# Kernel optimization log

Measured on AMD Instinct MI355X. Metric: run time of the kernel, lower is better.

Reference implementation:

```python
import jax, jax.numpy as jnp
import numpy as np

N = 4096      # number of nodes (seq_len); > 1000 so dag positional encoding is skipped
IN = 45       # input_dim
HID = 256     # hidden_dim
NH = 4        # num_heads
DH = HID // NH
E = 131072    # edges (avg degree 32)
# bucketed time bias: (lo, hi, weight)
BUCKETS = ((0.0, 5.0, 0.2), (5.0, 15.0, 0.1), (15.0, 60.0, 0.0), (60.0, 240.0, -0.1))
NEG = -1e9


def setup_inputs() -> dict:
    key = jax.random.key(0)
    ks = jax.random.split(key, 16)

    def lin_w(k, fan_in, fan_out):
        return (jax.random.normal(k, (fan_in, fan_out), jnp.float32) / np.float32(np.sqrt(fan_in)))

    return {
        "node_features": jax.random.normal(ks[0], (N, IN), jnp.float32),
        "temporal_data": jax.random.uniform(ks[1], (N, N, 2), jnp.float32) * 300.0,  # dt minutes in [0,300)
        "edge_index": jax.random.randint(ks[2], (2, E), 0, N),
        "W_in": lin_w(ks[3], IN, HID), "b_in": jnp.zeros((HID,), jnp.float32),
        "Wq": lin_w(ks[4], HID, HID), "bq": jnp.zeros((HID,), jnp.float32),
        "Wk": lin_w(ks[5], HID, HID), "bk": jnp.zeros((HID,), jnp.float32),
        "Wv": lin_w(ks[6], HID, HID), "bv": jnp.zeros((HID,), jnp.float32),
        "Wo": lin_w(ks[7], HID, HID), "bo": jnp.zeros((HID,), jnp.float32),
    }


def reference(node_features, temporal_data, edge_index, W_in, b_in, Wq, bq, Wk, bk, Wv, bv, Wo, bo):
    L = node_features.shape[0]
    x = node_features @ W_in + b_in                      # [L, HID]; pos-enc skipped since L > 1000

    def heads(W, b):
        return (x @ W + b).reshape(L, NH, DH).transpose(1, 0, 2)  # [NH, L, DH]

    q, k, v = heads(Wq, bq), heads(Wk, bk), heads(Wv, bv)

    scores = jnp.einsum('hld,hsd->hls', q, k) / np.float32(np.sqrt(DH))  # [NH, L, L]

    # bucketed time bias from dt_minutes
    dt = temporal_data[:, :, 0]
    tb = jnp.zeros_like(dt)
    for lo, hi, w in BUCKETS:
        tb = tb + np.float32(w) * ((dt >= lo) & (dt <= hi)).astype(dt.dtype)
    scores = scores + tb[None]                           # broadcast over heads

    # edge mask: True blocks attention; edges and self-loops allowed
    u, vdst = edge_index[0], edge_index[1]
    block = jnp.ones((L, L), dtype=bool).at[u, vdst].set(False)
    diag = jnp.arange(L)
    block = block.at[diag, diag].set(False)
    scores = jnp.where(block[None], NEG, scores)

    attn = jax.nn.softmax(scores, axis=-1)               # eval mode: no dropout
    out = jnp.einsum('hls,hsd->hld', attn, v)            # [NH, L, DH]
    out = out.transpose(1, 0, 2).reshape(L, HID)         # [L, HID]
    return out @ Wo + bo
```

## Files before the change

### kernel.cpp

```cpp
#include <hip/hip_runtime.h>
#include <hip/hip_bf16.h>
#include <stdint.h>

#define N_NODES 4096
#define HIDDEN 256
#define NHEAD 4
#define DHEAD 64
#define NEDGE 131072
#define MASK_WORDS 128
#define KIN 64
#define MAXDEG 1024

typedef __attribute__((ext_vector_type(8))) short bf16x8;
typedef __attribute__((ext_vector_type(4))) float f32x4;
typedef __hip_bfloat16 bf16;

__device__ __forceinline__ float b2f(unsigned short s) {
    union { float f; unsigned u; } x;
    x.u = ((unsigned)s) << 16;
    return x.f;
}
__device__ __forceinline__ unsigned short f2bu(float f) {
    bf16 b = __float2bfloat16(f);
    return *(unsigned short*)&b;
}

__global__ __launch_bounds__(256) void prep_kernel(
    const float* __restrict__ nf,
    const float* __restrict__ W_in, const float* __restrict__ b_in,
    const float* __restrict__ Wq, const float* __restrict__ bq,
    const float* __restrict__ Wk, const float* __restrict__ bk,
    const float* __restrict__ Wv, const float* __restrict__ bv,
    const float* __restrict__ Wo,
    unsigned int* __restrict__ mask, bf16* __restrict__ nfp,
    bf16* __restrict__ WqkvT, float* __restrict__ bqkv,
    bf16* __restrict__ WoT)
{
    int t = blockIdx.x * 256 + threadIdx.x;
    if (t < 131072) {
        ((uint4*)mask)[t] = make_uint4(0, 0, 0, 0);
        return;
    }
    t -= 131072;
    if (t < N_NODES * KIN) {
        int row = t >> 6, c = t & 63;
        float v = (c < 45) ? nf[row * 45 + c] : 0.f;
        nfp[t] = __float2bfloat16(v);
        return;
    }
    t -= N_NODES * KIN;
    if (t < 3 * 256 * KIN) {
        int which = t >> 14, r = t & 16383;
        int n = r & 255, kk = r >> 8;
        const float* W = (which == 0) ? Wq : (which == 1) ? Wk : Wv;
        float dot = 0.f;
        if (kk < 45) {
            const float* wrow = W_in + kk * 256;
            for (int c = 0; c < 256; ++c)
                dot += wrow[c] * W[c * 256 + n];
        }
        WqkvT[(size_t)which * 16384 + (size_t)n * KIN + kk] = __float2bfloat16(dot);
        return;
    }
    t -= 3 * 256 * KIN;
    if (t < 3 * 256) {
        int which = t >> 8, n = t & 255;
        const float* W = (which == 0) ? Wq : (which == 1) ? Wk : Wv;
        const float* b = (which == 0) ? bq : (which == 1) ? bk : bv;
        float acc = b[n];
        for (int c = 0; c < 256; ++c)
            acc += b_in[c] * W[c * 256 + n];
        bqkv[t] = acc;
        return;
    }
    t -= 3 * 256;
    if (t < 65536) {
        int kk = t >> 8, n = t & 255;
        WoT[(size_t)n * 256 + kk] = __float2bfloat16(Wo[(size_t)kk * 256 + n]);
    }
}

template <bool OUT_BF16>
__device__ __forceinline__ void gemm_body(
    const bf16* __restrict__ A, const bf16* __restrict__ Bt,
    const float* __restrict__ bias, void* __restrict__ Cv,
    int K, int m_base, int n0)
{
    const int lane = threadIdx.x & 63;
    const int row = lane & 15, quad = lane >> 4;
    f32x4 acc0 = {0.f, 0.f, 0.f, 0.f};
    f32x4 acc1 = {0.f, 0.f, 0.f, 0.f};
    const short* Ap = (const short*)A;
    const short* Bp = (const short*)Bt;

    for (int k0 = 0; k0 < K; k0 += 32) {
        bf16x8 b  = *(const bf16x8*)(Bp + (size_t)(n0 + row) * K + k0 + quad * 8);
        bf16x8 a0 = *(const bf16x8*)(Ap + (size_t)(m_base + row) * K + k0 + quad * 8);
        bf16x8 a1 = *(const bf16x8*)(Ap + (size_t)(m_base + 16 + row) * K + k0 + quad * 8);
        acc0 = __builtin_amdgcn_mfma_f32_16x16x32_bf16(a0, b, acc0, 0, 0, 0);
        acc1 = __builtin_amdgcn_mfma_f32_16x16x32_bf16(a1, b, acc1, 0, 0, 0);
    }

    const int col = row;
    const float bval = bias[n0 + col];
#pragma unroll
    for (int e = 0; e < 4; ++e) {
        int m0 = m_base + quad * 4 + e;
        int m1 = m0 + 16;
        float v0 = acc0[e] + bval;
        float v1 = acc1[e] + bval;
        if (OUT_BF16) {
            ((bf16*)Cv)[(size_t)m0 * HIDDEN + n0 + col] = __float2bfloat16(v0);
            ((bf16*)Cv)[(size_t)m1 * HIDDEN + n0 + col] = __float2bfloat16(v1);
        } else {
            ((float*)Cv)[(size_t)m0 * HIDDEN + n0 + col] = v0;
            ((float*)Cv)[(size_t)m1 * HIDDEN + n0 + col] = v1;
        }
    }
}

__global__ __launch_bounds__(256) void qkv_scatter_kernel(
    const bf16* __restrict__ nfp, const bf16* __restrict__ WqkvT,
    const float* __restrict__ bqkv, const int* __restrict__ eidx,
    float* __restrict__ q, bf16* __restrict__ k, bf16* __restrict__ v,
    unsigned int* __restrict__ mask)
{
    int bx = blockIdx.x;
    if (bx < 1536) {
        int ntile = bx >> 5, mrow = bx & 31;
        int which = ntile >> 4;
        const bf16* Bt = WqkvT + (size_t)which * 16384;
        const float* bias = bqkv + which * 256;
        int wave = threadIdx.x >> 6;
        int mb = mrow * 128 + wave * 32;
        int n0 = (ntile & 15) * 16;
        if (which == 0)      gemm_body<false>(nfp, Bt, bias, q, KIN, mb, n0);
        else if (which == 1) gemm_body<true>(nfp, Bt, bias, k, KIN, mb, n0);
        else                 gemm_body<true>(nfp, Bt, bias, v, KIN, mb, n0);
        return;
    }
    int t = (bx - 1536) * 256 + threadIdx.x;
    if (t < NEDGE) {
        int u = eidx[t], w = eidx[NEDGE + t];
        atomicOr(&mask[u * MASK_WORDS + (w >> 5)], 1u << (w & 31));
    } else {
        int i = t - NEDGE;
        if (i < N_NODES)
            atomicOr(&mask[i * MASK_WORDS + (i >> 5)], 1u << (i & 31));
    }
}

__global__ __launch_bounds__(256) void attn_kernel(
    const float* __restrict__ q, const bf16* __restrict__ k,
    const bf16* __restrict__ v, const float* __restrict__ temporal,
    const unsigned int* __restrict__ mask, bf16* __restrict__ att)
{
    __shared__ int jlist[MAXDEG];
    __shared__ float qs[HIDDEN];
    __shared__ float pj[NHEAD][64];
    __shared__ int cnt;
    const int i = blockIdx.x, tid = threadIdx.x;

    if (tid == 0) cnt = 0;
    qs[tid] = q[(size_t)i * HIDDEN + tid];
    __syncthreads();
    if (tid < MASK_WORDS) {
        unsigned int bits = mask[(size_t)i * MASK_WORDS + tid];
        int n = __popc(bits);
        if (n) {
            int pos = atomicAdd(&cnt, n);
            while (bits) {
                int b = __ffs(bits) - 1;
                bits &= bits - 1;
                if (pos < MAXDEG) jlist[pos] = (tid << 5) + b;
                ++pos;
            }
        }
    }
    __syncthreads();
    const int nn = cnt;

    const int h = tid >> 6, lane = tid & 63;
    const int half = lane >> 5, dpair = lane & 31;
    const float* trow = temporal + (size_t)i * N_NODES * 2;
    const unsigned short* kp = (const unsigned short*)k;
    const unsigned short* vp = (const unsigned short*)v;
    const float* qh = qs + h * DHEAD;

    float l = 0.f, acc0 = 0.f, acc1 = 0.f;

    for (int c0 = 0; c0 < nn; c0 += 64) {
        const int cend = min(64, nn - c0);
        float s = -3.0e38f;
        if (lane < cend) {
            int j = jlist[c0 + lane];
            float dt = trow[(size_t)j * 2];
            const unsigned short* krow = kp + (size_t)j * HIDDEN + h * DHEAD;
            bf16x8 k8[8];
#pragma unroll
            for (int t = 0; t < 8; ++t)
                k8[t] = *(const bf16x8*)(krow + t * 8);
            float dot = 0.f;
#pragma unroll
            for (int t = 0; t < 8; ++t)
#pragma unroll
                for (int e = 0; e < 8; ++e)
                    dot += b2f((unsigned short)k8[t][e]) * qh[t * 8 + e];
            float tb = 0.f;
            tb += 0.2f * (float)((dt >= 0.f)  & (dt <= 5.f));
            tb += 0.1f * (float)((dt >= 5.f)  & (dt <= 15.f));
            tb -= 0.1f * (float)((dt >= 60.f) & (dt <= 240.f));
            s = dot * 0.125f + tb;
        }
        float p = __expf(s);
        float csum = p;
#pragma unroll
        for (int off = 32; off >= 1; off >>= 1)
            csum += __shfl_xor(csum, off, 64);
        pj[h][lane] = p;
        l += csum;
        for (int u0 = 0; u0 < cend; u0 += 8) {
#pragma unroll
            for (int t = 0; t < 4; ++t) {
                int idx = u0 + 2 * t + half;
                bool valid = idx < cend;
                int j = jlist[c0 + (valid ? idx : 0)];
                float pv = valid ? pj[h][idx] : 0.f;
                const unsigned short* vrow = vp + (size_t)j * HIDDEN + h * DHEAD + dpair * 2;
                ushort2 v2 = *(const ushort2*)vrow;
                acc0 += pv * b2f(v2.x);
                acc1 += pv * b2f(v2.y);
            }
        }
    }

    acc0 += __shfl_xor(acc0, 32, 64);
    acc1 += __shfl_xor(acc1, 32, 64);
    if (half == 0) {
        ushort2 o;
        o.x = f2bu(acc0 / l);
        o.y = f2bu(acc1 / l);
        *(ushort2*)((unsigned short*)att + (size_t)i * HIDDEN + h * DHEAD + dpair * 2) = o;
    }
}

__global__ __launch_bounds__(256) void gemm_out_kernel(
    const bf16* __restrict__ att, const bf16* __restrict__ WoT,
    const float* __restrict__ bo, float* __restrict__ out)
{
    int wave = threadIdx.x >> 6;
    gemm_body<false>(att, WoT, bo, out, HIDDEN,
                     blockIdx.y * 128 + wave * 32, blockIdx.x * 16);
}

extern "C" void kernel_launch(void* const* d_in, const int* in_sizes, int n_in,
                              void* d_out, int out_size, void* d_ws, size_t ws_size,
                              hipStream_t stream) {
    const float* nf       = (const float*)d_in[0];
    const float* temporal = (const float*)d_in[1];
    const int*   eidx     = (const int*)  d_in[2];
    const float* W_in     = (const float*)d_in[3];
    const float* b_in     = (const float*)d_in[4];
    const float* Wq       = (const float*)d_in[5];
    const float* bq       = (const float*)d_in[6];
    const float* Wk       = (const float*)d_in[7];
    const float* bk       = (const float*)d_in[8];
    const float* Wv       = (const float*)d_in[9];
    const float* bv       = (const float*)d_in[10];
    const float* Wo       = (const float*)d_in[11];
    const float* bo       = (const float*)d_in[12];
    float* out = (float*)d_out;

    char* ws = (char*)d_ws;
    const size_t MiB = 1 << 20, KiB = 1 << 10;
    unsigned int* mask = (unsigned int*)(ws);
    bf16*  nfp   = (bf16*)(ws + 2 * MiB);
    bf16*  WqkvT = (bf16*)(ws + 2 * MiB + 512 * KiB);
    float* bqkv  = (float*)(ws + 2 * MiB + 640 * KiB);
    bf16*  WoT   = (bf16*)(ws + 3 * MiB);
    float* q     = (float*)(ws + 4 * MiB);
    bf16*  kb    = (bf16*)(ws + 8 * MiB);
    bf16*  vb    = (bf16*)(ws + 10 * MiB);
    bf16*  att   = (bf16*)(ws + 12 * MiB);

    {
        int total = 131072 + N_NODES * KIN + 3 * 256 * KIN + 3 * 256 + 65536;
        prep_kernel<<<(total + 255) / 256, 256, 0, stream>>>(
            nf, W_in, b_in, Wq, bq, Wk, bk, Wv, bv, Wo,
            mask, nfp, WqkvT, bqkv, WoT);
    }

    qkv_scatter_kernel<<<1536 + 528, 256, 0, stream>>>(
        nfp, WqkvT, bqkv, eidx, q, kb, vb, mask);

    attn_kernel<<<N_NODES, 256, 0, stream>>>(q, kb, vb, temporal, mask, att);

    gemm_out_kernel<<<dim3(16, 32), 256, 0, stream>>>(att, WoT, bo, out);
}
```

Measured before the change: 247.2 us.

## Restructure attention to one wave per query row, store Q as bf16

The attention kernel now gives each wavefront its own query row, four rows per block, instead of spreading one row across a whole 256-thread block. The neighbor list is built with a wave-level prefix scan rather than LDS atomics and block barriers. Each lane handles all four heads' dot products for its neighbor, and the V accumulation reads 4 contiguous bf16 values per lane, unrolled by 4. Q is also written and read in bf16 to halve its traffic. This trades fewer barriers and better V coalescing for more per-lane work on K loads and a smaller neighbor cap of 512.

```diff
diff --git a/kernel.cpp b/kernel.cpp
--- a/kernel.cpp
+++ b/kernel.cpp
@@ -9,7 +9,7 @@
 #define NEDGE 131072
 #define MASK_WORDS 128
 #define KIN 64
-#define MAXDEG 1024
+#define CAP 512
 
 typedef __attribute__((ext_vector_type(8))) short bf16x8;
 typedef __attribute__((ext_vector_type(4))) float f32x4;
@@ -122,7 +122,7 @@
 __global__ __launch_bounds__(256) void qkv_scatter_kernel(
     const bf16* __restrict__ nfp, const bf16* __restrict__ WqkvT,
     const float* __restrict__ bqkv, const int* __restrict__ eidx,
-    float* __restrict__ q, bf16* __restrict__ k, bf16* __restrict__ v,
+    bf16* __restrict__ q, bf16* __restrict__ k, bf16* __restrict__ v,
     unsigned int* __restrict__ mask)
 {
     int bx = blockIdx.x;
@@ -134,9 +134,8 @@
         int wave = threadIdx.x >> 6;
         int mb = mrow * 128 + wave * 32;
         int n0 = (ntile & 15) * 16;
-        if (which == 0)      gemm_body<false>(nfp, Bt, bias, q, KIN, mb, n0);
-        else if (which == 1) gemm_body<true>(nfp, Bt, bias, k, KIN, mb, n0);
-        else                 gemm_body<true>(nfp, Bt, bias, v, KIN, mb, n0);
+        bf16* C = (which == 0) ? q : (which == 1) ? k : v;
+        gemm_body<true>(nfp, Bt, bias, C, KIN, mb, n0);
         return;
     }
     int t = (bx - 1536) * 256 + threadIdx.x;
@@ -151,97 +150,133 @@
 }
 
 __global__ __launch_bounds__(256) void attn_kernel(
-    const float* __restrict__ q, const bf16* __restrict__ k,
+    const bf16* __restrict__ q, const bf16* __restrict__ k,
     const bf16* __restrict__ v, const float* __restrict__ temporal,
     const unsigned int* __restrict__ mask, bf16* __restrict__ att)
 {
-    __shared__ int jlist[MAXDEG];
-    __shared__ float qs[HIDDEN];
-    __shared__ float pj[NHEAD][64];
-    __shared__ int cnt;
-    const int i = blockIdx.x, tid = threadIdx.x;
-
-    if (tid == 0) cnt = 0;
-    qs[tid] = q[(size_t)i * HIDDEN + tid];
-    __syncthreads();
-    if (tid < MASK_WORDS) {
-        unsigned int bits = mask[(size_t)i * MASK_WORDS + tid];
-        int n = __popc(bits);
-        if (n) {
-            int pos = atomicAdd(&cnt, n);
-            while (bits) {
-                int b = __ffs(bits) - 1;
-                bits &= bits - 1;
-                if (pos < MAXDEG) jlist[pos] = (tid << 5) + b;
-                ++pos;
-            }
-        }
-    }
-    __syncthreads();
-    const int nn = cnt;
-
-    const int h = tid >> 6, lane = tid & 63;
-    const int half = lane >> 5, dpair = lane & 31;
+    __shared__ int   jl[4][CAP];
+    __shared__ float qsw[4][HIDDEN];
+    __shared__ float pch[4][4][68];
+    const int w    = threadIdx.x >> 6;
+    const int lane = threadIdx.x & 63;
+    const int i    = blockIdx.x * 4 + w;
+
+    {
+        const unsigned short* qp = (const unsigned short*)q + (size_t)i * HIDDEN + 4 * lane;
+        ushort4 q4 = *(const ushort4*)qp;
+        qsw[w][4 * lane + 0] = b2f(q4.x);
+        qsw[w][4 * lane + 1] = b2f(q4.y);
+        qsw[w][4 * lane + 2] = b2f(q4.z);
+        qsw[w][4 * lane + 3] = b2f(q4.w);
+    }
+
+    const unsigned int* mrow = mask + (size_t)i * MASK_WORDS;
+    unsigned int w0 = mrow[2 * lane], w1 = mrow[2 * lane + 1];
+    int c = __popc(w0) + __popc(w1);
+    int inc = c;
+#pragma unroll
+    for (int off = 1; off < 64; off <<= 1) {
+        int tt = __shfl_up(inc, off, 64);
+        if (lane >= off) inc += tt;
+    }
+    const int nn0 = __shfl(inc, 63, 64);
+    const int nn = (nn0 < CAP) ? nn0 : CAP;
+    int pos = inc - c;
+    int jb = lane * 64;
+    while (w0) {
+        int b = __ffs(w0) - 1; w0 &= w0 - 1;
+        if (pos < CAP) jl[w][pos] = jb + b;
+        ++pos;
+    }
+    jb += 32;
+    while (w1) {
+        int b = __ffs(w1) - 1; w1 &= w1 - 1;
+        if (pos < CAP) jl[w][pos] = jb + b;
+        ++pos;
+    }
+
     const float* trow = temporal + (size_t)i * N_NODES * 2;
     const unsigned short* kp = (const unsigned short*)k;
     const unsigned short* vp = (const unsigned short*)v;
-    const float* qh = qs + h * DHEAD;
-
-    float l = 0.f, acc0 = 0.f, acc1 = 0.f;
+    const int hsel = lane >> 4;
+
+    float l0 = 0.f, l1 = 0.f, l2 = 0.f, l3 = 0.f;
+    float a0 = 0.f, a1 = 0.f, a2 = 0.f, a3 = 0.f;
 
     for (int c0 = 0; c0 < nn; c0 += 64) {
         const int cend = min(64, nn - c0);
-        float s = -3.0e38f;
-        if (lane < cend) {
-            int j = jlist[c0 + lane];
+        int j = (lane < cend) ? jl[w][c0 + lane] : -1;
+        float tb = 0.f;
+        if (j >= 0) {
             float dt = trow[(size_t)j * 2];
-            const unsigned short* krow = kp + (size_t)j * HIDDEN + h * DHEAD;
-            bf16x8 k8[8];
-#pragma unroll
-            for (int t = 0; t < 8; ++t)
-                k8[t] = *(const bf16x8*)(krow + t * 8);
-            float dot = 0.f;
-#pragma unroll
-            for (int t = 0; t < 8; ++t)
-#pragma unroll
-                for (int e = 0; e < 8; ++e)
-                    dot += b2f((unsigned short)k8[t][e]) * qh[t * 8 + e];
-            float tb = 0.f;
             tb += 0.2f * (float)((dt >= 0.f)  & (dt <= 5.f));
             tb += 0.1f * (float)((dt >= 5.f)  & (dt <= 15.f));
             tb -= 0.1f * (float)((dt >= 60.f) & (dt <= 240.f));
-            s = dot * 0.125f + tb;
-        }
-        float p = __expf(s);
-        float csum = p;
-#pragma unroll
-        for (int off = 32; off >= 1; off >>= 1)
-            csum += __shfl_xor(csum, off, 64);
-        pj[h][lane] = p;
-        l += csum;
-        for (int u0 = 0; u0 < cend; u0 += 8) {
-#pragma unroll
-            for (int t = 0; t < 4; ++t) {
-                int idx = u0 + 2 * t + half;
-                bool valid = idx < cend;
-                int j = jlist[c0 + (valid ? idx : 0)];
-                float pv = valid ? pj[h][idx] : 0.f;
-                const unsigned short* vrow = vp + (size_t)j * HIDDEN + h * DHEAD + dpair * 2;
-                ushort2 v2 = *(const ushort2*)vrow;
-                acc0 += pv * b2f(v2.x);
-                acc1 += pv * b2f(v2.y);
+        }
+#pragma unroll
+        for (int h = 0; h < 4; ++h) {
+            float dot = 0.f;
+            if (j >= 0) {
+                const unsigned short* krow = kp + (size_t)j * HIDDEN + h * DHEAD;
+#pragma unroll
+                for (int t = 0; t < 8; ++t) {
+                    bf16x8 k8 = *(const bf16x8*)(krow + t * 8);
+                    f32x4 qa = *(const f32x4*)(&qsw[w][h * DHEAD + t * 8]);
+                    f32x4 qb = *(const f32x4*)(&qsw[w][h * DHEAD + t * 8 + 4]);
+                    dot += b2f((unsigned short)k8[0]) * qa[0];
+                    dot += b2f((unsigned short)k8[1]) * qa[1];
+                    dot += b2f((unsigned short)k8[2]) * qa[2];
+                    dot += b2f((unsigned short)k8[3]) * qa[3];
+                    dot += b2f((unsigned short)k8[4]) * qb[0];
+                    dot += b2f((unsigned short)k8[5]) * qb[1];
+                    dot += b2f((unsigned short)k8[6]) * qb[2];
+                    dot += b2f((unsigned short)k8[7]) * qb[3];
+                }
             }
-        }
-    }
-
-    acc0 += __shfl_xor(acc0, 32, 64);
-    acc1 += __shfl_xor(acc1, 32, 64);
-    if (half == 0) {
-        ushort2 o;
-        o.x = f2bu(acc0 / l);
-        o.y = f2bu(acc1 / l);
-        *(ushort2*)((unsigned short*)att + (size_t)i * HIDDEN + h * DHEAD + dpair * 2) = o;
-    }
+            float s = (j >= 0) ? dot * 0.125f + tb : -3.0e38f;
+            float p = __expf(s);
+            float cs = p;
+#pragma unroll
+            for (int off = 32; off >= 1; off >>= 1)
+                cs += __shfl_xor(cs, off, 64);
+            pch[w][h][lane] = p;
+            if (h == 0) l0 += cs; else if (h == 1) l1 += cs;
+            else if (h == 2) l2 += cs; else l3 += cs;
+        }
+        const float* ph = pch[w][hsel];
+        int jj = 0;
+        for (; jj + 4 <= cend; jj += 4) {
+            int ja = jl[w][c0 + jj],     jb2 = jl[w][c0 + jj + 1];
+            int jc = jl[w][c0 + jj + 2], jd  = jl[w][c0 + jj + 3];
+            float pa = ph[jj], pb = ph[jj + 1], pc = ph[jj + 2], pd = ph[jj + 3];
+            ushort4 va = *(const ushort4*)(vp + (size_t)ja  * HIDDEN + 4 * lane);
+            ushort4 vb = *(const ushort4*)(vp + (size_t)jb2 * HIDDEN + 4 * lane);
+            ushort4 vc = *(const ushort4*)(vp + (size_t)jc  * HIDDEN + 4 * lane);
+            ushort4 vd = *(const ushort4*)(vp + (size_t)jd  * HIDDEN + 4 * lane);
+            a0 += pa * b2f(va.x) + pb * b2f(vb.x) + pc * b2f(vc.x) + pd * b2f(vd.x);
+            a1 += pa * b2f(va.y) + pb * b2f(vb.y) + pc * b2f(vc.y) + pd * b2f(vd.y);
+            a2 += pa * b2f(va.z) + pb * b2f(vb.z) + pc * b2f(vc.z) + pd * b2f(vd.z);
+            a3 += pa * b2f(va.w) + pb * b2f(vb.w) + pc * b2f(vc.w) + pd * b2f(vd.w);
+        }
+        for (; jj < cend; ++jj) {
+            int jx = jl[w][c0 + jj];
+            float px = ph[jj];
+            ushort4 vx = *(const ushort4*)(vp + (size_t)jx * HIDDEN + 4 * lane);
+            a0 += px * b2f(vx.x);
+            a1 += px * b2f(vx.y);
+            a2 += px * b2f(vx.z);
+            a3 += px * b2f(vx.w);
+        }
+    }
+
+    float lsel = (hsel == 0) ? l0 : (hsel == 1) ? l1 : (hsel == 2) ? l2 : l3;
+    float inv = 1.f / lsel;
+    ushort4 o;
+    o.x = f2bu(a0 * inv);
+    o.y = f2bu(a1 * inv);
+    o.z = f2bu(a2 * inv);
+    o.w = f2bu(a3 * inv);
+    *(ushort4*)((unsigned short*)att + (size_t)i * HIDDEN + 4 * lane) = o;
 }
 
 __global__ __launch_bounds__(256) void gemm_out_kernel(
@@ -278,10 +313,10 @@
     bf16*  WqkvT = (bf16*)(ws + 2 * MiB + 512 * KiB);
     float* bqkv  = (float*)(ws + 2 * MiB + 640 * KiB);
     bf16*  WoT   = (bf16*)(ws + 3 * MiB);
-    float* q     = (float*)(ws + 4 * MiB);
-    bf16*  kb    = (bf16*)(ws + 8 * MiB);
-    bf16*  vb    = (bf16*)(ws + 10 * MiB);
-    bf16*  att   = (bf16*)(ws + 12 * MiB);
+    bf16*  qb    = (bf16*)(ws + 4 * MiB);
+    bf16*  kb    = (bf16*)(ws + 6 * MiB);
+    bf16*  vb    = (bf16*)(ws + 8 * MiB);
+    bf16*  att   = (bf16*)(ws + 10 * MiB);
 
     {
         int total = 131072 + N_NODES * KIN + 3 * 256 * KIN + 3 * 256 + 65536;
@@ -291,9 +326,9 @@
     }
 
     qkv_scatter_kernel<<<1536 + 528, 256, 0, stream>>>(
-        nfp, WqkvT, bqkv, eidx, q, kb, vb, mask);
-
-    attn_kernel<<<N_NODES, 256, 0, stream>>>(q, kb, vb, temporal, mask, att);
+        nfp, WqkvT, bqkv, eidx, qb, kb, vb, mask);
+
+    attn_kernel<<<N_NODES / 4, 256, 0, stream>>>(qb, kb, vb, temporal, mask, att);
 
     gemm_out_kernel<<<dim3(16, 32), 256, 0, stream>>>(att, WoT, bo, out);
 }
```

New measurement: 243.9 us. No clear change (-1.3%).
